# Kernel tuning notes

Hardware: AMD Instinct MI355X
Metric: run time of the kernel (lower is better)

## Reference

```python
import jax, jax.numpy as jnp
import numpy as np

N_CLASSES = 43
G = 4            # n_grid
N_ITER = 3
EPS = 1e-5


def _conv(x, w, b, stride, pad):
    y = jax.lax.conv_general_dilated(
        x, w, (stride, stride), [(pad, pad), (pad, pad)],
        dimension_numbers=("NCHW", "OIHW", "NCHW"))
    return y + b[None, :, None, None]


def _bn(x, gamma, beta):
    # training-mode batch norm (batch statistics, biased variance)
    m = jnp.mean(x, axis=(0, 2, 3), keepdims=True)
    v = jnp.mean((x - m) ** 2, axis=(0, 2, 3), keepdims=True)
    xh = (x - m) * jax.lax.rsqrt(v + EPS)
    return xh * gamma[None, :, None, None] + beta[None, :, None, None]


def _lrelu(x):
    return jnp.where(x >= 0, x, 0.1 * x)


def _squash(v):
    sn = jnp.sum(v * v, axis=-1, keepdims=True)
    return (sn / (1.0 + sn)) * v / jnp.sqrt(sn)


def setup_inputs() -> dict:
    key = jax.random.key(0)
    ks = jax.random.split(key, 24)
    f32 = jnp.float32
    d = {}
    d["x"] = jax.random.normal(ks[0], (8, 3, 128, 128), dtype=f32)
    # conv backbone params (He-ish scale)
    def w(k, shape, fan_in):
        return jax.random.normal(k, shape, dtype=f32) * (1.0 / np.sqrt(fan_in))
    d["c1w"] = w(ks[1], (128, 3, 3, 3), 3 * 9);   d["c1b"] = jnp.zeros((128,), f32)
    d["g1"] = jnp.ones((128,), f32);              d["b1"] = jnp.zeros((128,), f32)
    d["c2w"] = w(ks[2], (256, 128, 3, 3), 128 * 9); d["c2b"] = jnp.zeros((256,), f32)
    d["g2"] = jnp.ones((256,), f32);              d["b2"] = jnp.zeros((256,), f32)
    d["c3w"] = w(ks[3], (64, 256, 4, 4), 256 * 16); d["c3b"] = jnp.zeros((64,), f32)
    d["g3"] = jnp.ones((64,), f32);               d["b3"] = jnp.zeros((64,), f32)
    d["c4w"] = w(ks[4], (128, 64, 4, 4), 64 * 16);  d["c4b"] = jnp.zeros((128,), f32)
    d["g4"] = jnp.ones((128,), f32);              d["b4"] = jnp.zeros((128,), f32)
    d["c5w"] = w(ks[5], (256, 128, 4, 4), 128 * 16); d["c5b"] = jnp.zeros((256,), f32)
    d["g5"] = jnp.ones((256,), f32);              d["b5"] = jnp.zeros((256,), f32)
    # route weights: torch shape (1, n_nodes, n_caps, in_C, out_C); drop leading 1
    d["rw"] = 0.1 * jax.random.normal(ks[6], (512, N_CLASSES, 8, 21), dtype=f32)
    return d


def reference(x, c1w, c1b, g1, b1, c2w, c2b, g2, b2, c3w, c3b, g3, b3,
              c4w, c4b, g4, b4, c5w, c5b, g5, b5, rw):
    B = x.shape[0]
    h = _lrelu(_bn(_conv(x, c1w, c1b, 1, 1), g1, b1))
    h = _lrelu(_bn(_conv(h, c2w, c2b, 1, 1), g2, b2))
    h = _lrelu(_bn(_conv(h, c3w, c3b, 2, 1), g3, b3))
    h = _lrelu(_bn(_conv(h, c4w, c4b, 2, 1), g4, b4))
    h = _lrelu(_bn(_conv(h, c5w, c5b, 2, 1), g5, b5))  # [B,256,4G,4G]
    # view(B,256,4,4*G^2) -> chunk G^2 along last -> per chunk permute(0,2,3,1).view(B,512,8), stack chunks first
    y = h.reshape(B, 256, 4, G * G, 4)                # (B,C,h,chunk,w)
    y = jnp.transpose(y, (3, 0, 2, 4, 1))             # (G^2,B,h,w,C)
    caps_in = y.reshape(G * G * B, 512, 8)            # B' = G^2*B
    # priors: [B',n_nodes,n_caps,out_C]
    priors = jnp.einsum("bni,nkio->bnko", caps_in, rw)
    logits = jnp.zeros_like(priors)
    outputs = None
    for i in range(N_ITER):
        probs = jax.nn.softmax(logits, axis=2)
        s = jnp.sum(probs * priors, axis=1, keepdims=True)  # [B',1,k,21]
        outputs = _squash(s)
        if i != N_ITER - 1:
            logits = logits + jnp.sum(priors * outputs, axis=-1, keepdims=True)
    out = outputs[:, 0]                               # [B',k,21]
    out = out.reshape(G, G, B, N_CLASSES, 21)
    return jnp.transpose(out, (2, 0, 1, 3, 4))        # [B,G,G,k,21]
```

## Files before the change

kernel.cpp:

```cpp
#include <hip/hip_runtime.h>
#include <math.h>

typedef unsigned int   uint;
typedef unsigned short ushort;
using bf16x8 = __attribute__((ext_vector_type(8))) __bf16;
using f32x4  = __attribute__((ext_vector_type(4))) float;

constexpr int NB   = 128;
constexpr int NCAP = 512;
constexpr int NCLS = 43;
constexpr int NO   = 21;
constexpr int KO   = NCLS * NO;

constexpr size_t F_X1H  = 0;
constexpr size_t F_PART = 0;
constexpr size_t F_STAT = 16777216;
constexpr size_t F_WPH  = 16778240;
constexpr size_t F_WPL  = 16925696;
constexpr size_t F_W3H  = 17073152;
constexpr size_t F_W3L  = 17204224;
constexpr size_t F_W4H  = 17335296;
constexpr size_t F_W4L  = 17400832;
constexpr size_t F_W5H  = 17466368;
constexpr size_t F_W5L  = 17728512;
constexpr size_t F_X3H  = 17990656;
constexpr size_t F_H3   = 51545088;
constexpr size_t F_X4H  = 53642240;
constexpr size_t F_H4   = 55739392;
constexpr size_t F_X5H  = 56787968;
constexpr size_t F_H5   = 57836544;
constexpr size_t F_PRI  = 0;
constexpr size_t F_CAPS = 59179008;
constexpr size_t F_LOG  = 59703296;
constexpr size_t F_S    = 65339392;
constexpr size_t F_OUTS = 65454976;
constexpr size_t F_ZERO = 65570560;

__device__ inline ushort f2bf(float x) {
  uint u = __float_as_uint(x);
  uint r = (u + 0x7fffu + ((u >> 16) & 1u)) >> 16;
  return (ushort)r;
}
__device__ inline float bf2f(ushort h) { return __uint_as_float(((uint)h) << 16); }

#define GLL16(gsrc, ldst)                                               \
  __builtin_amdgcn_global_load_lds(                                     \
      (const __attribute__((address_space(1))) void*)(gsrc),            \
      (__attribute__((address_space(3))) void*)(ldst), 16, 0, 0)

__global__ __launch_bounds__(256) void conv1_k(
    const float* __restrict__ in, const float* __restrict__ w,
    ushort* __restrict__ oh, float* __restrict__ stats)
{
  constexpr int KS = 3, ICC = 3, IHT = 10, IWT = 18;
  const int ocb = blockIdx.z & 3;
  const int b   = blockIdx.z >> 2;
  const int tx0 = blockIdx.x * 16;
  const int ty0 = blockIdx.y * 8;
  const int oc0 = ocb * 32;

  __shared__ float lin[ICC][IHT][IWT];
  __shared__ float lw[ICC][KS * KS][32];
  __shared__ float b1sum[32], b1sq[32];

  const int t  = threadIdx.x;
  const int pq = t & 3;
  const int ty = (t >> 2) & 7;
  const int oq = t >> 5;

  float acc[4][4];
#pragma unroll
  for (int m = 0; m < 4; ++m)
#pragma unroll
    for (int j = 0; j < 4; ++j) acc[m][j] = 0.f;

  const int gx0 = tx0 - 1;
  const int gy0 = ty0 - 1;

  for (int e = t; e < ICC * IHT * IWT; e += 256) {
    int ic = e / (IHT * IWT);
    int rr = e % (IHT * IWT);
    int ey = rr / IWT, ex = rr % IWT;
    int gy = gy0 + ey, gx = gx0 + ex;
    float v = 0.f;
    if ((unsigned)gy < 128u && (unsigned)gx < 128u)
      v = in[((size_t)(b * 3 + ic) * 128 + gy) * 128 + gx];
    lin[ic][ey][ex] = v;
  }
  for (int e = t; e < ICC * 9 * 32; e += 256) {
    int ocl = e & 31;
    int rr  = e >> 5;
    int kk  = rr % 9;
    int ic  = rr / 9;
    lw[ic][kk][ocl] = w[((size_t)(oc0 + ocl) * 3 + ic) * 9 + kk];
  }
  __syncthreads();

  for (int ic = 0; ic < ICC; ++ic) {
#pragma unroll
    for (int ky = 0; ky < KS; ++ky) {
#pragma unroll
      for (int kx = 0; kx < KS; ++kx) {
        float xv[4];
#pragma unroll
        for (int j = 0; j < 4; ++j)
          xv[j] = lin[ic][ty + ky][pq * 4 + j + kx];
        const float4 w4 = *(const float4*)&lw[ic][ky * KS + kx][oq * 4];
#pragma unroll
        for (int j = 0; j < 4; ++j) {
          acc[0][j] = fmaf(w4.x, xv[j], acc[0][j]);
          acc[1][j] = fmaf(w4.y, xv[j], acc[1][j]);
          acc[2][j] = fmaf(w4.z, xv[j], acc[2][j]);
          acc[3][j] = fmaf(w4.w, xv[j], acc[3][j]);
        }
      }
    }
  }

  const int oy = ty0 + ty;
  const int oc0q = oc0 + oq * 4;
  const size_t icb = oc0q >> 3;
  const int off = oc0q & 7;
  float sm[4] = {0.f, 0.f, 0.f, 0.f}, qm[4] = {0.f, 0.f, 0.f, 0.f};
#pragma unroll
  for (int j = 0; j < 4; ++j) {
    int px = tx0 + pq * 4 + j;
    size_t pxg = ((size_t)b * 128 + oy) * 128 + px;
    size_t addr = (icb * 131072 + pxg) * 8 + off;
    ushort h0 = f2bf(acc[0][j]);
    ushort h1 = f2bf(acc[1][j]);
    ushort h2 = f2bf(acc[2][j]);
    ushort h3 = f2bf(acc[3][j]);
    uint2 uh; uh.x = (uint)h0 | ((uint)h1 << 16); uh.y = (uint)h2 | ((uint)h3 << 16);
    *(uint2*)(oh + addr) = uh;
    float v0 = bf2f(h0), v1 = bf2f(h1), v2 = bf2f(h2), v3 = bf2f(h3);
    sm[0] += v0; qm[0] += v0 * v0;
    sm[1] += v1; qm[1] += v1 * v1;
    sm[2] += v2; qm[2] += v2 * v2;
    sm[3] += v3; qm[3] += v3 * v3;
  }
#pragma unroll
  for (int o = 16; o > 0; o >>= 1) {
#pragma unroll
    for (int m = 0; m < 4; ++m) {
      sm[m] += __shfl_xor(sm[m], o);
      qm[m] += __shfl_xor(qm[m], o);
    }
  }
  if ((t & 31) == 0) {
#pragma unroll
    for (int m = 0; m < 4; ++m) { b1sum[oq * 4 + m] = sm[m]; b1sq[oq * 4 + m] = qm[m]; }
  }
  __syncthreads();
  if (t < 32) {
    atomicAdd(&stats[oc0 + t], b1sum[t]);
    atomicAdd(&stats[128 + oc0 + t], b1sq[t]);
  }
}

__global__ __launch_bounds__(256) void bn_apply_x1_k(
    ushort* __restrict__ xh, const float* __restrict__ stats,
    const float* __restrict__ g, const float* __restrict__ bt)
{
  __shared__ float scs[128], sfs[128];
  const int t = threadIdx.x;
  if (t < 128) {
    float m = stats[t] * (1.f / 131072.f);
    float v = stats[128 + t] * (1.f / 131072.f) - m * m;
    float rs = rsqrtf(v + 1e-5f);
    float sc = g[t] * rs;
    scs[t] = sc; sfs[t] = bt[t] - m * sc;
  }
  __syncthreads();
  const size_t total = (size_t)16 * 131072;
  const size_t stride = (size_t)gridDim.x * 256;
  for (size_t i = (size_t)blockIdx.x * 256 + t; i < total; i += stride) {
    int j = (int)(i >> 17);
    int c0 = j * 8;
    uint4 vh = *(const uint4*)(xh + i * 8);
    uint hw[4] = {vh.x, vh.y, vh.z, vh.w};
    uint ohv[4];
#pragma unroll
    for (int m = 0; m < 4; ++m) {
      float f0 = __uint_as_float(hw[m] << 16);
      float f1 = __uint_as_float(hw[m] & 0xffff0000u);
      float a0 = fmaf(f0, scs[c0 + 2*m],   sfs[c0 + 2*m]);   a0 = fmaxf(a0, 0.1f * a0);
      float a1 = fmaf(f1, scs[c0 + 2*m+1], sfs[c0 + 2*m+1]); a1 = fmaxf(a1, 0.1f * a1);
      ohv[m] = (uint)f2bf(a0) | ((uint)f2bf(a1) << 16);
    }
    uint4 rh = {ohv[0], ohv[1], ohv[2], ohv[3]};
    *(uint4*)(xh + i * 8) = rh;
  }
}

__global__ __launch_bounds__(256) void bn_stats_nhwc_k(
    const float* __restrict__ x, float* __restrict__ stats,
    int cmask, int lg2c, int totpx)
{
  int g = blockIdx.x * 256 + threadIdx.x;
  int c = g & cmask;
  int p0 = g >> lg2c;
  int stride = (gridDim.x * 256) >> lg2c;
  float s = 0.f, q = 0.f;
  for (int p = p0; p < totpx; p += stride) {
    float v = x[((size_t)p << lg2c) | c];
    s += v; q += v * v;
  }
  atomicAdd(&stats[c], s);
  atomicAdd(&stats[cmask + 1 + c], q);
}

template<int C>
__global__ __launch_bounds__(256) void split_blocked_k(
    const float* __restrict__ h, const float* __restrict__ stats,
    const float* __restrict__ g, const float* __restrict__ bt, float inv_n,
    ushort* __restrict__ oh, int totpx)
{
  __shared__ ushort lh[16][C + 8];
  __shared__ float scs[C], sfs[C];
  const int px0 = blockIdx.x * 16;
  const int t = threadIdx.x;
  if (t < C) {
    float m = stats[t] * inv_n;
    float v = stats[C + t] * inv_n - m * m;
    float rs = rsqrtf(v + 1e-5f);
    float sc = g[t] * rs;
    scs[t] = sc; sfs[t] = bt[t] - m * sc;
  }
  __syncthreads();
  for (int e = t; e < 16 * C / 4; e += 256) {
    int px = e / (C / 4);
    int c0 = (e % (C / 4)) * 4;
    float4 v  = *(const float4*)(h + (size_t)(px0 + px) * C + c0);
    float a0 = fmaf(v.x, scs[c0],   sfs[c0]);   a0 = fmaxf(a0, 0.1f * a0);
    float a1 = fmaf(v.y, scs[c0+1], sfs[c0+1]); a1 = fmaxf(a1, 0.1f * a1);
    float a2 = fmaf(v.z, scs[c0+2], sfs[c0+2]); a2 = fmaxf(a2, 0.1f * a2);
    float a3 = fmaf(v.w, scs[c0+3], sfs[c0+3]); a3 = fmaxf(a3, 0.1f * a3);
    lh[px][c0]   = f2bf(a0);
    lh[px][c0+1] = f2bf(a1);
    lh[px][c0+2] = f2bf(a2);
    lh[px][c0+3] = f2bf(a3);
  }
  __syncthreads();
  for (int e = t; e < 16 * (C / 8); e += 256) {
    int j = e >> 4, px = e & 15;
    *(uint4*)(oh + ((size_t)j * totpx + px0 + px) * 8) = *(const uint4*)&lh[px][j * 8];
  }
}

__global__ void wsplit_all_k(
    const float* __restrict__ c2w, const float* __restrict__ c3w,
    const float* __restrict__ c4w, const float* __restrict__ c5w,
    ushort* __restrict__ wph, ushort* __restrict__ wpl,
    ushort* __restrict__ w3h, ushort* __restrict__ w3l,
    ushort* __restrict__ w4h, ushort* __restrict__ w4l,
    ushort* __restrict__ w5h, ushort* __restrict__ w5l)
{
  int i = blockIdx.x * 256 + threadIdx.x;
  if (i < 294912) {
    int kk = i % 9; int r = i / 9; int ic = r & 127; int oc = r >> 7;
    float v = c2w[i];
    ushort hi = f2bf(v), lo = f2bf(v - bf2f(hi));
    int ohf = oc >> 7, of = (oc >> 4) & 7, lr = oc & 15;
    int ic32 = ic >> 5, kg = (ic >> 3) & 3, ici = ic & 7;
    size_t d = ((((size_t)(kk * 4 + ic32) * 2 + ohf) * 8 + of) * 4 + kg) * 128
               + lr * 8 + ici;
    wph[d] = hi; wpl[d] = lo;
    return;
  }
  i -= 294912;
  const float* w; ushort *wh, *wl; int OC, IC, n;
  if (i < 262144)      { w = c3w; wh = w3h; wl = w3l; OC = 64;  IC = 256; n = i; }
  else if (i < 393216) { w = c4w; wh = w4h; wl = w4l; OC = 128; IC = 64;  n = i - 262144; }
  else if (i < 917504) { w = c5w; wh = w5h; wl = w5l; OC = 256; IC = 128; n = i - 393216; }
  else return;
  int kx = n & 3, ky = (n >> 2) & 3;
  int ic = (n >> 4) % IC, oc = (n >> 4) / IC;
  float v = w[n];
  ushort hi = f2bf(v), lo = f2bf(v - bf2f(hi));
  int NCH = IC >> 3, NWO = OC >> 6;
  int wo = oc >> 6, of = (oc >> 4) & 3, lr = oc & 15;
  int ch = ic >> 3, ici = ic & 7;
  size_t d = ((((size_t)(ky * NCH + ch) * NWO + wo) * 4 + of) * 4 + kx) * 128
             + lr * 8 + ici;
  wh[d] = hi; wl[d] = lo;
}

__device__ __forceinline__ void stage_x(
    const ushort* __restrict__ x1h, const ushort* __restrict__ zbuf,
    ushort* dst, int t, int b, int gy, int ic32)
{
  const bool rowok = (unsigned)gy < 128u;
  const size_t rowb = ((size_t)b * 128 + (rowok ? gy : 0)) * 128;
#pragma unroll
  for (int k = 0; k < 2; ++k) {
    int e = t + k * 256;
    int icg = e / 130;
    int xi = e - icg * 130;
    int gx = xi - 1;
    const ushort* sh = zbuf;
    if (rowok && (unsigned)gx < 128u) {
      size_t gi = ((size_t)(ic32 * 4 + icg) * 131072 + rowb + gx) * 8;
      sh = x1h + gi;
    }
    GLL16(sh, dst + (size_t)e * 8);
  }
  if (t < 8) {
    int e = 512 + t;
    int xi = e - 390;
    int gx = xi - 1;
    const ushort* sh = zbuf;
    if (rowok && (unsigned)gx < 128u) {
      size_t gi = ((size_t)(ic32 * 4 + 3) * 131072 + rowb + gx) * 8;
      sh = x1h + gi;
    }
    GLL16(sh, dst + (size_t)e * 8);
  }
}

__global__ __launch_bounds__(256, 2) void conv2_mfma_k(
    const ushort* __restrict__ x1h,
    const ushort* __restrict__ wph, const ushort* __restrict__ wpl,
    const ushort* __restrict__ zbuf, float* __restrict__ stats2,
    ushort* __restrict__ x3h)
{
  const int bid = blockIdx.x;
  const int wid = (bid & 7) * 128 + (bid >> 3);
  const int y0  = wid & 127;
  const int b   = wid >> 7;

  __shared__ ushort xs[2][4][130][8];
  __shared__ float bsum[2][256], bsq[2][256];

  const int t = threadIdx.x;
  const int w  = t >> 6;
  const int l  = t & 63;
  const int xhf = w & 1;
  const int ohf = w >> 1;
  const int lr = l & 15;
  const int kg = l >> 4;

  f32x4 acc[8][4];
#pragma unroll
  for (int i = 0; i < 8; ++i)
#pragma unroll
    for (int j = 0; j < 4; ++j) acc[i][j] = (f32x4){0.f, 0.f, 0.f, 0.f};

  stage_x(x1h, zbuf, (ushort*)&xs[0][0][0][0], t, b, y0 - 1, 0);
  __syncthreads();

  for (int ky = 0; ky < 3; ++ky) {
    for (int ic32 = 0; ic32 < 4; ++ic32) {
      const int buf = ic32 & 1;
      const int np = ky * 4 + ic32 + 1;
      if (np < 12) {
        stage_x(x1h, zbuf, (ushort*)&xs[buf ^ 1][0][0][0],
                t, b, y0 + (np >> 2) - 1, np & 3);
      }
#pragma unroll
      for (int kx = 0; kx < 3; ++kx) {
        const int kk = ky * 3 + kx;
        const size_t wbase =
            ((size_t)((kk * 4 + ic32) * 2 + ohf)) * 4096 + (size_t)l * 8;
        const ushort* pwh = wph + wbase;
        const ushort* pwl = wpl + wbase;

        bf16x8 xbh[4];
#pragma unroll
        for (int pf = 0; pf < 4; ++pf) {
          int xi = xhf * 64 + pf * 16 + lr + kx;
          xbh[pf] = *(const bf16x8*)&xs[buf][kg][xi][0];
        }
#pragma unroll
        for (int oh2 = 0; oh2 < 2; ++oh2) {
          bf16x8 awh[4], awl[4];
#pragma unroll
          for (int o4 = 0; o4 < 4; ++o4) {
            awh[o4] = *(const bf16x8*)(pwh + (oh2 * 4 + o4) * 512);
            awl[o4] = *(const bf16x8*)(pwl + (oh2 * 4 + o4) * 512);
          }
#pragma unroll
          for (int o4 = 0; o4 < 4; ++o4) {
            const int of = oh2 * 4 + o4;
#pragma unroll
            for (int pf = 0; pf < 4; ++pf) {
              acc[of][pf] = __builtin_amdgcn_mfma_f32_16x16x32_bf16(awh[o4], xbh[pf], acc[of][pf], 0, 0, 0);
              acc[of][pf] = __builtin_amdgcn_mfma_f32_16x16x32_bf16(awl[o4], xbh[pf], acc[of][pf], 0, 0, 0);
            }
          }
        }
      }
      __syncthreads();
    }
  }

#pragma unroll
  for (int of = 0; of < 8; ++of) {
    float s4[4] = {0.f, 0.f, 0.f, 0.f}, q4[4] = {0.f, 0.f, 0.f, 0.f};
#pragma unroll
    for (int pf = 0; pf < 4; ++pf) {
      int oc = ohf * 128 + of * 16 + kg * 4;
      int x  = xhf * 64 + pf * 16 + lr;
      size_t pxg = ((size_t)b * 128 + y0) * 128 + x;
      size_t base = ((size_t)(oc >> 3) * 131072 + pxg) * 8 + (oc & 7);
      f32x4 a = acc[of][pf];
      ushort h0 = f2bf(a[0]);
      ushort h1 = f2bf(a[1]);
      ushort h2 = f2bf(a[2]);
      ushort h3 = f2bf(a[3]);
      uint2 uh; uh.x = (uint)h0 | ((uint)h1 << 16); uh.y = (uint)h2 | ((uint)h3 << 16);
      *(uint2*)(x3h + base) = uh;
      float v0 = bf2f(h0), v1 = bf2f(h1), v2 = bf2f(h2), v3 = bf2f(h3);
      s4[0] += v0; q4[0] += v0 * v0;
      s4[1] += v1; q4[1] += v1 * v1;
      s4[2] += v2; q4[2] += v2 * v2;
      s4[3] += v3; q4[3] += v3 * v3;
    }
#pragma unroll
    for (int o = 8; o > 0; o >>= 1) {
#pragma unroll
      for (int j = 0; j < 4; ++j) {
        s4[j] += __shfl_xor(s4[j], o);
        q4[j] += __shfl_xor(q4[j], o);
      }
    }
    if (lr == 0) {
      int oc = ohf * 128 + of * 16 + kg * 4;
#pragma unroll
      for (int j = 0; j < 4; ++j) { bsum[xhf][oc + j] = s4[j]; bsq[xhf][oc + j] = q4[j]; }
    }
  }
  __syncthreads();
  if (t < 256) {
    atomicAdd(&stats2[t],       bsum[0][t] + bsum[1][t]);
    atomicAdd(&stats2[256 + t], bsq[0][t] + bsq[1][t]);
  }
}

template<int IC, int OC, int OH, int OW, int WPX, int CS, bool FBN>
__global__ __launch_bounds__(256, 2) void convs_mfma_k(
    const ushort* __restrict__ xh,
    const ushort* __restrict__ wh, const ushort* __restrict__ wl,
    const float* __restrict__ stats, const float* __restrict__ gg,
    const float* __restrict__ bb, float inv_n,
    float* __restrict__ part)
{
  constexpr int IH  = 2 * OH, IW = 2 * OW;
  constexpr int NCH = IC / 8;
  constexpr int NCHB = NCH / CS;
  constexpr int PFX = OW / 16;
  constexpr int RW  = 4 / WPX;
  constexpr int NZ = 4 * CS;
  constexpr int NX = OH / 4;
  constexpr int NWO = OC / 64;
  constexpr int SBN = FBN ? IC : 1;

  const int bid = blockIdx.x;
  const int wid = (bid & 7) * (NZ * NX) + (bid >> 3);
  const int zi = wid % NZ;
  const int y0 = ((wid / NZ) % NX) * 4;
  const int b  = wid / (NZ * NX);
  const int ky = zi & 3;
  const int cs = zi >> 2;

  __shared__ ushort xs[4][2][OW + 2][8];
  __shared__ float scs[SBN], sfs[SBN];

  const int t = threadIdx.x;
  if (FBN) {
    for (int c = t; c < IC; c += 256) {
      float m = stats[c] * inv_n;
      float v = stats[IC + c] * inv_n - m * m;
      float rs = rsqrtf(v + 1e-5f);
      float sc = gg[c] * rs;
      scs[c] = sc; sfs[c] = bb[c] - m * sc;
    }
  }

  const int w = t >> 6, l = t & 63;
  const int wo = w / WPX, wp = w % WPX;
  const int lr = l & 15, kg = l >> 4;
  const int oc0w = wo * 64;
  const int rb = wp * RW;

  f32x4 acc[4][4];
#pragma unroll
  for (int i = 0; i < 4; ++i)
#pragma unroll
    for (int j = 0; j < 4; ++j) acc[i][j] = (f32x4){0.f, 0.f, 0.f, 0.f};

  for (int cc = 0; cc < NCHB; ++cc) {
    const int ch = cs * NCHB + cc;
    __syncthreads();
    for (int e = t; e < 4 * (IW + 2); e += 256) {
      int r  = e / (IW + 2);
      int xi = e % (IW + 2);
      int xp = xi - 1;
      int iy = 2 * (y0 + r) + ky - 1;
      uint4 rh = {0, 0, 0, 0};
      if ((unsigned)iy < (unsigned)IH && (unsigned)xp < (unsigned)IW) {
        size_t gi = ((((size_t)ch * 8 + b) * IH + iy) * IW + xp) * 8;
        uint4 vh = *(const uint4*)(xh + gi);
        if (FBN) {
          int c0 = ch * 8;
          uint hw[4] = {vh.x, vh.y, vh.z, vh.w};
          uint ohv[4];
#pragma unroll
          for (int m = 0; m < 4; ++m) {
            float f0 = __uint_as_float(hw[m] << 16);
            float f1 = __uint_as_float(hw[m] & 0xffff0000u);
            float a0 = fmaf(f0, scs[c0 + 2*m],   sfs[c0 + 2*m]);   a0 = fmaxf(a0, 0.1f * a0);
            float a1 = fmaf(f1, scs[c0 + 2*m+1], sfs[c0 + 2*m+1]); a1 = fmaxf(a1, 0.1f * a1);
            ohv[m] = (uint)f2bf(a0) | ((uint)f2bf(a1) << 16);
          }
          rh.x = ohv[0]; rh.y = ohv[1]; rh.z = ohv[2]; rh.w = ohv[3];
        } else {
          rh = vh;
        }
      }
      int par = xp & 1;
      int idx = (xp + 1) >> 1;
      *(uint4*)&xs[r][par][idx][0] = rh;
    }
    __syncthreads();

    const size_t wbase =
        ((size_t)(ky * NCH + ch) * NWO + wo) * 2048 + (size_t)l * 8;
    bf16x8 ah[4], al[4], bh[4];
#pragma unroll
    for (int of = 0; of < 4; ++of) {
      ah[of] = *(const bf16x8*)(wh + wbase + of * 512);
      al[of] = *(const bf16x8*)(wl + wbase + of * 512);
    }
    const int par = 1 - (kg & 1);
    const int xoff = kg >> 1;
#pragma unroll
    for (int pf = 0; pf < 4; ++pf) {
      int row = rb + pf / PFX;
      int x   = (pf % PFX) * 16 + lr;
      bh[pf] = *(const bf16x8*)&xs[row][par][x + xoff][0];
    }
#pragma unroll
    for (int of = 0; of < 4; ++of) {
#pragma unroll
      for (int pf = 0; pf < 4; ++pf) {
        acc[of][pf] = __builtin_amdgcn_mfma_f32_16x16x32_bf16(ah[of], bh[pf], acc[of][pf], 0, 0, 0);
        acc[of][pf] = __builtin_amdgcn_mfma_f32_16x16x32_bf16(al[of], bh[pf], acc[of][pf], 0, 0, 0);
      }
    }
  }

  float* yp = part + (size_t)zi * (8 * OH * OW * OC);
#pragma unroll
  for (int of = 0; of < 4; ++of) {
#pragma unroll
    for (int pf = 0; pf < 4; ++pf) {
      int row = rb + pf / PFX;
      int x   = (pf % PFX) * 16 + lr;
      int oc  = oc0w + of * 16 + kg * 4;
      float* p = yp + (((size_t)b * OH + y0 + row) * OW + x) * OC + oc;
      f32x4 a = acc[of][pf];
      float4 v = {a[0], a[1], a[2], a[3]};
      *(float4*)p = v;
    }
  }
}

__global__ __launch_bounds__(256) void reduce_k(
    const float* __restrict__ part, float* __restrict__ h,
    int n4, int nparts)
{
  int i = blockIdx.x * 256 + threadIdx.x;
  if (i >= n4) return;
  float4 a = ((const float4*)part)[i];
  for (int z = 1; z < nparts; ++z) {
    float4 b = ((const float4*)part)[(size_t)z * n4 + i];
    a.x += b.x; a.y += b.y; a.z += b.z; a.w += b.w;
  }
  ((float4*)h)[i] = a;
}

__global__ void caps_k(const float* __restrict__ h5, const float* __restrict__ stats,
                       const float* __restrict__ g5, const float* __restrict__ b5,
                       float* __restrict__ caps)
{
  int e = blockIdx.x * 256 + threadIdx.x;
  if (e >= NB * NCAP * 8) return;
  int ii = e & 7;
  int n  = (e >> 3) & 511;
  int jb = e >> 12;
  int j = jb >> 3, b = jb & 7;
  int i = n >> 7, k = (n >> 5) & 3, ch = ((n & 31) << 3) | ii;
  int hh = (i << 2) | (j >> 2);
  int ww = ((j & 3) << 2) | k;
  float m  = stats[ch] * (1.f / 2048.f);
  float vv = stats[256 + ch] * (1.f / 2048.f) - m * m;
  float rs = rsqrtf(vv + 1e-5f);
  float sc = g5[ch] * rs;
  float sf = b5[ch] - m * sc;
  float v = h5[(((size_t)b * 16 + hh) * 16 + ww) * 256 + ch];
  float a = fmaf(v, sc, sf);
  a = fmaxf(a, 0.1f * a);
  caps[e] = a;
}

__global__ __launch_bounds__(256) void priors_k(
    const float* __restrict__ caps, const float* __restrict__ rw,
    ushort* __restrict__ priors)
{
  const int n = blockIdx.x;
  __shared__ float lrw[NCLS * 8 * NO];
  __shared__ float lc[NB * 8];
  const int t = threadIdx.x;
  for (int e = t; e < NCLS * 8 * NO; e += 256)
    lrw[e] = rw[(size_t)n * NCLS * 8 * NO + e];
  for (int e = t; e < NB * 8; e += 256) {
    int b = e >> 3, ii = e & 7;
    lc[e] = caps[((size_t)b * NCAP + n) * 8 + ii];
  }
  __syncthreads();

  int p[4], kk[4], oo[4];
#pragma unroll
  for (int q = 0; q < 4; ++q) {
    p[q]  = t + q * 256;
    kk[q] = (p[q] < KO) ? p[q] / NO : 0;
    oo[q] = (p[q] < KO) ? p[q] % NO : 0;
  }
  for (int b = 0; b < NB; ++b) {
    const float* cb = &lc[b * 8];
    float c0 = cb[0], c1 = cb[1], c2 = cb[2], c3 = cb[3];
    float c4 = cb[4], c5 = cb[5], c6 = cb[6], c7 = cb[7];
    ushort* pout = priors + ((size_t)b * NCAP + n) * KO;
#pragma unroll
    for (int q = 0; q < 4; ++q) {
      if (p[q] < KO) {
        const float* wv = &lrw[kk[q] * (8 * NO) + oo[q]];
        float a = c0 * wv[0];
        a = fmaf(c1, wv[21],  a);
        a = fmaf(c2, wv[42],  a);
        a = fmaf(c3, wv[63],  a);
        a = fmaf(c4, wv[84],  a);
        a = fmaf(c5, wv[105], a);
        a = fmaf(c6, wv[126], a);
        a = fmaf(c7, wv[147], a);
        pout[p[q]] = f2bf(a);
      }
    }
  }
}

__global__ __launch_bounds__(256) void route_s_partial(
    const ushort* __restrict__ priors, float* __restrict__ s)
{
  const int b  = blockIdx.x >> 3;
  const int ns = blockIdx.x & 7;
  const int t  = threadIdx.x;
  const int p0 = t, p1 = t + 256, p2 = t + 512, p3 = t + 768;
  float a0 = 0.f, a1 = 0.f, a2 = 0.f, a3 = 0.f;
  const ushort* pb = priors + ((size_t)b * NCAP + ns * 64) * KO;
#pragma unroll 2
  for (int n = 0; n < 64; ++n) {
    const ushort* pn = pb + (size_t)n * KO;
    a0 += bf2f(pn[p0]); a1 += bf2f(pn[p1]); a2 += bf2f(pn[p2]);
    if (p3 < KO) a3 += bf2f(pn[p3]);
  }
  const float sc = 1.f / 43.f;
  atomicAdd(&s[b * KO + p0], a0 * sc);
  atomicAdd(&s[b * KO + p1], a1 * sc);
  atomicAdd(&s[b * KO + p2], a2 * sc);
  if (p3 < KO) atomicAdd(&s[b * KO + p3], a3 * sc);
}

__global__ __launch_bounds__(256) void route_iter_k(
    const ushort* __restrict__ priors, const float* __restrict__ souts,
    float* __restrict__ logits, float* __restrict__ s,
    int readPrev, int writeL)
{
  const int b  = blockIdx.x >> 3;
  const int ns = blockIdx.x & 7;
  const int t  = threadIdx.x;
  const int w  = t >> 6;
  const int lane = t & 63;
  const bool act = lane < NCLS;

  __shared__ float prow[4][928];

  float so[NO], sacc[NO], v[NO];
  if (act) {
#pragma unroll
    for (int o = 0; o < NO; ++o) so[o] = souts[b * KO + lane * NO + o];
  }
#pragma unroll
  for (int o = 0; o < NO; ++o) { sacc[o] = 0.f; v[o] = 0.f; }

  for (int nn = 0; nn < 16; ++nn) {
    const int n = ns * 64 + w * 16 + nn;
    const ushort* pr = priors + ((size_t)(b * NCAP + n)) * KO;
#pragma unroll
    for (int q = 0; q < 15; ++q) {
      int e = lane + q * 64;
      if (e < KO) prow[w][e] = bf2f(pr[e]);
    }
    float L = -1e30f;
    if (act) {
      float d = 0.f;
#pragma unroll
      for (int o = 0; o < NO; ++o) v[o] = prow[w][lane * NO + o];
#pragma unroll
      for (int o = 0; o < NO; ++o) d = fmaf(v[o], so[o], d);
      size_t lidx = ((size_t)(b * NCAP + n)) * NCLS + lane;
      L = (readPrev ? logits[lidx] : 0.f) + d;
      if (writeL) logits[lidx] = L;
    }
    float m = L;
#pragma unroll
    for (int off = 32; off > 0; off >>= 1) m = fmaxf(m, __shfl_xor(m, off));
    float ex = act ? __expf(L - m) : 0.f;
    float sm = ex;
#pragma unroll
    for (int off = 32; off > 0; off >>= 1) sm += __shfl_xor(sm, off);
    float pk = ex / sm;
    if (act) {
#pragma unroll
      for (int o = 0; o < NO; ++o) sacc[o] = fmaf(pk, v[o], sacc[o]);
    }
  }
  if (act) {
#pragma unroll
    for (int o = 0; o < NO; ++o) prow[w][lane * NO + o] = sacc[o];
  }
  __syncthreads();
  for (int e = t; e < KO; e += 256)
    atomicAdd(&s[b * KO + e], prow[0][e] + prow[1][e] + prow[2][e] + prow[3][e]);
}

__global__ void squash_k(const float* __restrict__ s, float* __restrict__ souts)
{
  int i = blockIdx.x * 256 + threadIdx.x;
  if (i >= NB * NCLS) return;
  int b = i / NCLS, k = i % NCLS;
  const float* sv = s + b * KO + k * NO;
  float sn = 0.f;
#pragma unroll
  for (int o = 0; o < NO; ++o) sn += sv[o] * sv[o];
  float f = sqrtf(sn) / (1.f + sn);
  float* ov = souts + b * KO + k * NO;
#pragma unroll
  for (int o = 0; o < NO; ++o) ov[o] = sv[o] * f;
}

__global__ void out_k(const float* __restrict__ souts, float* __restrict__ out)
{
  int i = blockIdx.x * 256 + threadIdx.x;
  if (i >= 8 * 16 * NCLS * NO) return;
  int o = i % NO;
  int r = i / NO;
  int k = r % NCLS; r /= NCLS;
  int g1 = r & 3; r >>= 2;
  int g0 = r & 3;
  int b  = r >> 2;
  int j  = g0 * 4 + g1;
  int jb = j * 8 + b;
  out[i] = souts[jb * KO + k * NO + o];
}

extern "C" void kernel_launch(void* const* d_in, const int* in_sizes, int n_in,
                              void* d_out, int out_size, void* d_ws, size_t ws_size,
                              hipStream_t stream)
{
  const float* x   = (const float*)d_in[0];
  const float* c1w = (const float*)d_in[1];
  const float* g1  = (const float*)d_in[3];  const float* b1  = (const float*)d_in[4];
  const float* c2w = (const float*)d_in[5];
  const float* g2  = (const float*)d_in[7];  const float* b2  = (const float*)d_in[8];
  const float* c3w = (const float*)d_in[9];
  const float* g3  = (const float*)d_in[11]; const float* b3  = (const float*)d_in[12];
  const float* c4w = (const float*)d_in[13];
  const float* g4  = (const float*)d_in[15]; const float* b4  = (const float*)d_in[16];
  const float* c5w = (const float*)d_in[17];
  const float* g5  = (const float*)d_in[19]; const float* b5  = (const float*)d_in[20];
  const float* rw  = (const float*)d_in[21];

  float* ws  = (float*)d_ws;
  float* out = (float*)d_out;

  ushort* x1h = (ushort*)(ws + F_X1H);
  ushort* wph = (ushort*)(ws + F_WPH);
  ushort* wpl = (ushort*)(ws + F_WPL);
  ushort* w3h = (ushort*)(ws + F_W3H);
  ushort* w3l = (ushort*)(ws + F_W3L);
  ushort* w4h = (ushort*)(ws + F_W4H);
  ushort* w4l = (ushort*)(ws + F_W4L);
  ushort* w5h = (ushort*)(ws + F_W5H);
  ushort* w5l = (ushort*)(ws + F_W5L);
  ushort* x3h = (ushort*)(ws + F_X3H);
  ushort* x4h = (ushort*)(ws + F_X4H);
  ushort* x5h = (ushort*)(ws + F_X5H);
  float* part   = ws + F_PART;
  float* h3     = ws + F_H3;
  float* h4     = ws + F_H4;
  float* h5     = ws + F_H5;
  float* caps   = ws + F_CAPS;
  ushort* priors = (ushort*)(ws + F_PRI);
  float* logits = ws + F_LOG;
  float* sbuf   = ws + F_S;
  float* souts  = ws + F_OUTS;
  float* stats  = ws + F_STAT;
  float* stats2 = ws + F_STAT + 512;
  ushort* zbuf  = (ushort*)(ws + F_ZERO);

  hipMemsetAsync(stats, 0, 1024 * sizeof(float), stream);
  hipMemsetAsync(zbuf, 0, 64, stream);

  wsplit_all_k<<<(1212416 + 255) / 256, 256, 0, stream>>>(
      c2w, c3w, c4w, c5w, wph, wpl, w3h, w3l, w4h, w4l, w5h, w5l);

  conv1_k<<<dim3(8, 16, 32), 256, 0, stream>>>(x, c1w, x1h, stats);

  bn_apply_x1_k<<<2048, 256, 0, stream>>>(x1h, stats, g1, b1);

  conv2_mfma_k<<<1024, 256, 0, stream>>>(x1h, wph, wpl, zbuf, stats2, x3h);

  convs_mfma_k<256, 64, 64, 64, 4, 1, true><<<512, 256, 0, stream>>>(
      x3h, w3h, w3l, stats2, g2, b2, 1.f / 131072.f, part);
  reduce_k<<<(524288 + 255) / 256, 256, 0, stream>>>(part, h3, 524288, 4);
  hipMemsetAsync(stats, 0, 2 * 64 * sizeof(float), stream);
  bn_stats_nhwc_k<<<256, 256, 0, stream>>>(h3, stats, 63, 6, 32768);
  split_blocked_k<64><<<2048, 256, 0, stream>>>(h3, stats, g3, b3, 1.f / 32768.f, x4h, 32768);

  convs_mfma_k<64, 128, 32, 32, 2, 2, false><<<512, 256, 0, stream>>>(
      x4h, w4h, w4l, stats, g4, b4, 0.f, part);
  reduce_k<<<(262144 + 255) / 256, 256, 0, stream>>>(part, h4, 262144, 8);
  hipMemsetAsync(stats, 0, 2 * 128 * sizeof(float), stream);
  bn_stats_nhwc_k<<<128, 256, 0, stream>>>(h4, stats, 127, 7, 8192);
  split_blocked_k<128><<<512, 256, 0, stream>>>(h4, stats, g4, b4, 1.f / 8192.f, x5h, 8192);

  convs_mfma_k<128, 256, 16, 16, 1, 2, false><<<256, 256, 0, stream>>>(
      x5h, w5h, w5l, stats, g5, b5, 0.f, part);
  reduce_k<<<(131072 + 255) / 256, 256, 0, stream>>>(part, h5, 131072, 8);
  hipMemsetAsync(stats, 0, 2 * 256 * sizeof(float), stream);
  bn_stats_nhwc_k<<<64, 256, 0, stream>>>(h5, stats, 255, 8, 2048);

  caps_k<<<2048, 256, 0, stream>>>(h5, stats, g5, b5, caps);
  priors_k<<<512, 256, 0, stream>>>(caps, rw, priors);

  hipMemsetAsync(sbuf, 0, NB * KO * sizeof(float), stream);
  route_s_partial<<<NB * 8, 256, 0, stream>>>(priors, sbuf);
  squash_k<<<(NB * NCLS + 255) / 256, 256, 0, stream>>>(sbuf, souts);

  hipMemsetAsync(sbuf, 0, NB * KO * sizeof(float), stream);
  route_iter_k<<<NB * 8, 256, 0, stream>>>(priors, souts, logits, sbuf, 0, 1);
  squash_k<<<(NB * NCLS + 255) / 256, 256, 0, stream>>>(sbuf, souts);

  hipMemsetAsync(sbuf, 0, NB * KO * sizeof(float), stream);
  route_iter_k<<<NB * 8, 256, 0, stream>>>(priors, souts, logits, sbuf, 1, 0);
  squash_k<<<(NB * NCLS + 255) / 256, 256, 0, stream>>>(sbuf, souts);

  out_k<<<(8 * 16 * NCLS * NO + 255) / 256, 256, 0, stream>>>(souts, out);
}
```

Measured before the change: 592.5 us.

## Split conv2 output channels across two blocks to raise occupancy

Each conv2 block now computes 128 of the 256 output channels instead of all 256, which doubles the grid to 2048 blocks and halves the per-thread accumulator array. Launch bounds rise to allow three blocks per CU, aiming to hide memory and LDS latency with more waves in flight. The cost is that the input row tile is staged into LDS twice (once per channel half), and BN-statistic atomics are spread over twice as many blocks.

```diff
diff --git a/kernel.cpp b/kernel.cpp
--- a/kernel.cpp
+++ b/kernel.cpp
@@ -318,19 +318,20 @@
   }
 }
 
-__global__ __launch_bounds__(256, 2) void conv2_mfma_k(
+__global__ __launch_bounds__(256, 3) void conv2_mfma_k(
     const ushort* __restrict__ x1h,
     const ushort* __restrict__ wph, const ushort* __restrict__ wpl,
     const ushort* __restrict__ zbuf, float* __restrict__ stats2,
     ushort* __restrict__ x3h)
 {
   const int bid = blockIdx.x;
-  const int wid = (bid & 7) * 128 + (bid >> 3);
-  const int y0  = wid & 127;
-  const int b   = wid >> 7;
+  const int wid = (bid & 7) * 256 + (bid >> 3);
+  const int ohT = wid & 1;
+  const int y0  = (wid >> 1) & 127;
+  const int b   = wid >> 8;
 
   __shared__ ushort xs[2][4][130][8];
-  __shared__ float bsum[2][256], bsq[2][256];
+  __shared__ float bsum[2][128], bsq[2][128];
 
   const int t = threadIdx.x;
   const int w  = t >> 6;
@@ -340,9 +341,9 @@
   const int lr = l & 15;
   const int kg = l >> 4;
 
-  f32x4 acc[8][4];
-#pragma unroll
-  for (int i = 0; i < 8; ++i)
+  f32x4 acc[4][4];
+#pragma unroll
+  for (int i = 0; i < 4; ++i)
 #pragma unroll
     for (int j = 0; j < 4; ++j) acc[i][j] = (f32x4){0.f, 0.f, 0.f, 0.f};
 
@@ -361,7 +362,7 @@
       for (int kx = 0; kx < 3; ++kx) {
         const int kk = ky * 3 + kx;
         const size_t wbase =
-            ((size_t)((kk * 4 + ic32) * 2 + ohf)) * 4096 + (size_t)l * 8;
+            ((size_t)((kk * 4 + ic32) * 2 + ohT)) * 4096 + (size_t)l * 8;
         const ushort* pwh = wph + wbase;
         const ushort* pwl = wpl + wbase;
 
@@ -372,21 +373,13 @@
           xbh[pf] = *(const bf16x8*)&xs[buf][kg][xi][0];
         }
 #pragma unroll
-        for (int oh2 = 0; oh2 < 2; ++oh2) {
-          bf16x8 awh[4], awl[4];
-#pragma unroll
-          for (int o4 = 0; o4 < 4; ++o4) {
-            awh[o4] = *(const bf16x8*)(pwh + (oh2 * 4 + o4) * 512);
-            awl[o4] = *(const bf16x8*)(pwl + (oh2 * 4 + o4) * 512);
-          }
-#pragma unroll
-          for (int o4 = 0; o4 < 4; ++o4) {
-            const int of = oh2 * 4 + o4;
-#pragma unroll
-            for (int pf = 0; pf < 4; ++pf) {
-              acc[of][pf] = __builtin_amdgcn_mfma_f32_16x16x32_bf16(awh[o4], xbh[pf], acc[of][pf], 0, 0, 0);
-              acc[of][pf] = __builtin_amdgcn_mfma_f32_16x16x32_bf16(awl[o4], xbh[pf], acc[of][pf], 0, 0, 0);
-            }
+        for (int o4 = 0; o4 < 4; ++o4) {
+          bf16x8 awh = *(const bf16x8*)(pwh + (ohf * 4 + o4) * 512);
+          bf16x8 awl = *(const bf16x8*)(pwl + (ohf * 4 + o4) * 512);
+#pragma unroll
+          for (int pf = 0; pf < 4; ++pf) {
+            acc[o4][pf] = __builtin_amdgcn_mfma_f32_16x16x32_bf16(awh, xbh[pf], acc[o4][pf], 0, 0, 0);
+            acc[o4][pf] = __builtin_amdgcn_mfma_f32_16x16x32_bf16(awl, xbh[pf], acc[o4][pf], 0, 0, 0);
           }
         }
       }
@@ -395,11 +388,11 @@
   }
 
 #pragma unroll
-  for (int of = 0; of < 8; ++of) {
+  for (int of = 0; of < 4; ++of) {
     float s4[4] = {0.f, 0.f, 0.f, 0.f}, q4[4] = {0.f, 0.f, 0.f, 0.f};
 #pragma unroll
     for (int pf = 0; pf < 4; ++pf) {
-      int oc = ohf * 128 + of * 16 + kg * 4;
+      int oc = ohT * 128 + ohf * 64 + of * 16 + kg * 4;
       int x  = xhf * 64 + pf * 16 + lr;
       size_t pxg = ((size_t)b * 128 + y0) * 128 + x;
       size_t base = ((size_t)(oc >> 3) * 131072 + pxg) * 8 + (oc & 7);
@@ -425,15 +418,15 @@
       }
     }
     if (lr == 0) {
-      int oc = ohf * 128 + of * 16 + kg * 4;
-#pragma unroll
-      for (int j = 0; j < 4; ++j) { bsum[xhf][oc + j] = s4[j]; bsq[xhf][oc + j] = q4[j]; }
+      int ocl = ohf * 64 + of * 16 + kg * 4;
+#pragma unroll
+      for (int j = 0; j < 4; ++j) { bsum[xhf][ocl + j] = s4[j]; bsq[xhf][ocl + j] = q4[j]; }
     }
   }
   __syncthreads();
-  if (t < 256) {
-    atomicAdd(&stats2[t],       bsum[0][t] + bsum[1][t]);
-    atomicAdd(&stats2[256 + t], bsq[0][t] + bsq[1][t]);
+  if (t < 128) {
+    atomicAdd(&stats2[ohT * 128 + t],       bsum[0][t] + bsum[1][t]);
+    atomicAdd(&stats2[256 + ohT * 128 + t], bsq[0][t] + bsq[1][t]);
   }
 }
 
@@ -820,7 +813,7 @@
 
   bn_apply_x1_k<<<2048, 256, 0, stream>>>(x1h, stats, g1, b1);
 
-  conv2_mfma_k<<<1024, 256, 0, stream>>>(x1h, wph, wpl, zbuf, stats2, x3h);
+  conv2_mfma_k<<<2048, 256, 0, stream>>>(x1h, wph, wpl, zbuf, stats2, x3h);
 
   convs_mfma_k<256, 64, 64, 64, 4, 1, true><<<512, 256, 0, stream>>>(
       x3h, w3h, w3l, stats2, g2, b2, 1.f / 131072.f, part);
```

Measured after the change: 614.1 us. 1.04x slower.
